# Kernel optimization log

Hardware: AMD Instinct MI355X
Metric: run time of the kernel (lower is better)

Reference implementation:

```python
import jax, jax.numpy as jnp
import numpy as np

D_MODEL = 1024
D_HIDDEN = 4096
BATCH = 4
SEQ = 2048
EPS = 1e-5
SLOPE = 0.01  # LeakyReLU default negative_slope


def layer_norm(x, g, b):
    m = jnp.mean(x, axis=-1, keepdims=True)
    v = jnp.mean(jnp.square(x - m), axis=-1, keepdims=True)
    return (x - m) * jax.lax.rsqrt(v + EPS) * g + b


def leaky_relu(x):
    return jnp.where(x >= 0, x, SLOPE * x)


def setup_inputs() -> dict:
    key = jax.random.key(0)
    ks = jax.random.split(key, 8)
    scale = D_MODEL ** 0.5
    x = jax.random.normal(ks[0], (BATCH, SEQ, D_MODEL), dtype=jnp.float32)
    qk = jax.random.normal(ks[1], (D_MODEL, D_MODEL), dtype=jnp.float32) / scale
    ov = jax.random.normal(ks[2], (D_MODEL, D_MODEL), dtype=jnp.float32) / scale
    ln1_g = jnp.ones((D_MODEL,), jnp.float32)
    ln1_b = jnp.zeros((D_MODEL,), jnp.float32)
    ln2_g = jnp.ones((D_MODEL,), jnp.float32)
    ln2_b = jnp.zeros((D_MODEL,), jnp.float32)
    # nn.Linear default init: uniform(-1/sqrt(fan_in), 1/sqrt(fan_in))
    def lin(k, fan_in, fan_out):
        k1, k2 = jax.random.split(k)
        bd = 1.0 / np.sqrt(fan_in)
        W = jax.random.uniform(k1, (fan_out, fan_in), jnp.float32, -bd, bd)
        b = jax.random.uniform(k2, (fan_out,), jnp.float32, -bd, bd)
        return W, b
    W_up, b_up = lin(ks[3], D_MODEL, D_HIDDEN)
    W_h, b_h = lin(ks[4], D_HIDDEN, D_HIDDEN)
    W_down, b_down = lin(ks[5], D_HIDDEN, D_MODEL)
    return {"x": x, "qk": qk, "ov": ov, "ln1_g": ln1_g, "ln1_b": ln1_b,
            "ln2_g": ln2_g, "ln2_b": ln2_b, "W_up": W_up, "b_up": b_up,
            "W_h": W_h, "b_h": b_h, "W_down": W_down, "b_down": b_down}


def reference(x, qk, ov, ln1_g, ln1_b, ln2_g, ln2_b,
              W_up, b_up, W_h, b_h, W_down, b_down):
    scale = D_MODEL ** 0.5
    # --- attention on ln1(x) ---
    h = layer_norm(x, ln1_g, ln1_b)                     # [B,S,D]
    scores = jnp.einsum('bsd,de,bte->bst', h, qk, h) / scale  # [B,S,S]
    n = h.shape[1]
    causal = jnp.tril(jnp.ones((n, n), bool))
    scores = jnp.where(causal, scores, -jnp.inf)
    probs = jax.nn.softmax(scores, axis=-1)
    attn = jnp.einsum('bst,btd,de->bse', probs, h, ov)  # [B,S,D]
    x = x + attn
    # --- MLP on ln2(x) ---
    h2 = layer_norm(x, ln2_g, ln2_b)
    a = leaky_relu(h2 @ W_up.T + b_up)
    a = leaky_relu(a @ W_h.T + b_h)
    a = leaky_relu(a @ W_down.T + b_down)
    return x + a
```

## Files before the change

### kernel.cpp

```cpp
#include <hip/hip_runtime.h>
#include <stdint.h>


typedef __attribute__((ext_vector_type(4))) float  f32x4;
typedef __attribute__((ext_vector_type(8))) __bf16 bf16v8;
typedef __attribute__((ext_vector_type(8))) unsigned short u16x8;
typedef unsigned short ushort_t;
typedef unsigned int   u32;

#define SLOPE 0.01f

__device__ __forceinline__ ushort_t f2bf(float f) {
  u32 u = __builtin_bit_cast(u32, f);
  u32 r = (u + 0x7FFFu + ((u >> 16) & 1u)) >> 16;
  return (ushort_t)r;
}
__device__ __forceinline__ float bf2f(ushort_t b) {
  u32 u = ((u32)b) << 16;
  return __builtin_bit_cast(float, u);
}

__device__ __forceinline__ void gload_lds16(const void* g, void* l) {
  __builtin_amdgcn_global_load_lds(
      (const __attribute__((address_space(1))) u32*)g,
      (__attribute__((address_space(3))) u32*)l, 16, 0, 0);
}

template<int EPI>
__global__ __launch_bounds__(512, 1)
void gemm_nt8(const ushort_t* __restrict__ A, const ushort_t* __restrict__ B,
              void* __restrict__ Cv, const float* __restrict__ bias,
              int M, int N, int K)
{
  extern __shared__ char smem[];
  const ushort_t* lds = (const ushort_t*)smem;
  const int tid = threadIdx.x;
  const int l   = tid & 63;
  const int m0 = blockIdx.y * 256;
  const int n0 = blockIdx.x * 256;
  const int wid = tid >> 6;
  const int wm = (wid >> 2) * 128;
  const int wn = (wid & 3) * 64;
  const int nt = K >> 6;

  const int  sg      = (((tid & 3) ^ ((tid >> 3) & 3))) * 8;
  const long rowA0   = (long)(m0 +       (tid >> 2)) * K;
  const long rowA1   = (long)(m0 + 128 + (tid >> 2)) * K;
  const long rowB0   = (long)(n0 +       (tid >> 2)) * K;
  const long rowB1   = (long)(n0 + 128 + (tid >> 2)) * K;
  const int  wbase16 = (tid & ~63) * 16;

#define STAGE_BOTH(TT) do {                                                   \
    const int  _buf = (TT) & 1;                                               \
    const long _k   = (long)(TT) * 64;                                        \
    char* _ra0 = (char*)smem + (_buf * 4 + 0) * 16384 + wbase16;              \
    char* _ra1 = (char*)smem + (_buf * 4 + 1) * 16384 + wbase16;              \
    char* _rb0 = (char*)smem + (_buf * 4 + 2) * 16384 + wbase16;              \
    char* _rb1 = (char*)smem + (_buf * 4 + 3) * 16384 + wbase16;              \
    gload_lds16(A + rowA0 + _k + sg,      _ra0);                              \
    gload_lds16(A + rowA1 + _k + sg,      _ra0 + 8192);                       \
    gload_lds16(B + rowB0 + _k + sg,      _rb0);                              \
    gload_lds16(B + rowB1 + _k + sg,      _rb0 + 8192);                       \
    gload_lds16(A + rowA0 + _k + 32 + sg, _ra1);                              \
    gload_lds16(A + rowA1 + _k + 32 + sg, _ra1 + 8192);                       \
    gload_lds16(B + rowB0 + _k + 32 + sg, _rb1);                              \
    gload_lds16(B + rowB1 + _k + 32 + sg, _rb1 + 8192);                       \
  } while (0)

  const int fr  = l & 15;
  const int fsl = (((l >> 4) ^ ((l >> 1) & 3))) * 8;

  f32x4 acc[8][4] = {};

  STAGE_BOTH(0);
  asm volatile("s_waitcnt vmcnt(4)" ::: "memory");
  __builtin_amdgcn_s_barrier();
  __builtin_amdgcn_sched_barrier(0);

  for (int t = 0; t < nt; ++t) {
    const int buf = t & 1;

    {
      const ushort_t* rA = lds + (buf * 4 + 0) * 8192 + (wm + fr) * 32 + fsl;
      const ushort_t* rB = lds + (buf * 4 + 2) * 8192 + (wn + fr) * 32 + fsl;
      bf16v8 av[8], bv[4];
#pragma unroll
      for (int mf = 0; mf < 8; mf++) av[mf] = *(const bf16v8*)(rA + mf * 512);
#pragma unroll
      for (int nf = 0; nf < 4; nf++) bv[nf] = *(const bf16v8*)(rB + nf * 512);

      if (t + 1 < nt) STAGE_BOTH(t + 1);

      __builtin_amdgcn_s_setprio(1);
#pragma unroll
      for (int mf = 0; mf < 8; mf++)
#pragma unroll
        for (int nf = 0; nf < 4; nf++)
          acc[mf][nf] = __builtin_amdgcn_mfma_f32_16x16x32_bf16(
              av[mf], bv[nf], acc[mf][nf], 0, 0, 0);
      __builtin_amdgcn_s_setprio(0);

      if (t + 1 < nt) {
        asm volatile("s_waitcnt vmcnt(8)" ::: "memory");
      } else {
        asm volatile("s_waitcnt vmcnt(0)" ::: "memory");
      }
      __builtin_amdgcn_s_barrier();
      __builtin_amdgcn_sched_barrier(0);
    }

    {
      const ushort_t* rA = lds + (buf * 4 + 1) * 8192 + (wm + fr) * 32 + fsl;
      const ushort_t* rB = lds + (buf * 4 + 3) * 8192 + (wn + fr) * 32 + fsl;
      bf16v8 av[8], bv[4];
#pragma unroll
      for (int mf = 0; mf < 8; mf++) av[mf] = *(const bf16v8*)(rA + mf * 512);
#pragma unroll
      for (int nf = 0; nf < 4; nf++) bv[nf] = *(const bf16v8*)(rB + nf * 512);

      __builtin_amdgcn_s_setprio(1);
#pragma unroll
      for (int mf = 0; mf < 8; mf++)
#pragma unroll
        for (int nf = 0; nf < 4; nf++)
          acc[mf][nf] = __builtin_amdgcn_mfma_f32_16x16x32_bf16(
              av[mf], bv[nf], acc[mf][nf], 0, 0, 0);
      __builtin_amdgcn_s_setprio(0);

      if (t + 1 < nt) {
        asm volatile("s_waitcnt vmcnt(4)" ::: "memory");
        __builtin_amdgcn_s_barrier();
        __builtin_amdgcn_sched_barrier(0);
      }
    }
  }
#undef STAGE_BOTH

  const int lr = (l >> 4) * 4;
#pragma unroll
  for (int mf = 0; mf < 8; mf++) {
    const int row0 = m0 + wm + mf * 16 + lr;
#pragma unroll
    for (int nf = 0; nf < 4; nf++) {
      const int col = n0 + wn + nf * 16 + fr;
      const float bcol = bias ? bias[col] : 0.f;
#pragma unroll
      for (int r = 0; r < 4; r++) {
        float v = acc[mf][nf][r];
        if constexpr (EPI == 2) {
          v += bcol;
          v = v >= 0.f ? v : SLOPE * v;
          ((ushort_t*)Cv)[(long)(row0 + r) * N + col] = f2bf(v);
        } else {
          ((ushort_t*)Cv)[(long)(row0 + r) * N + col] = f2bf(v);
        }
      }
    }
  }
}

template<int EPI, bool CAUSAL, bool KLIM>
__global__ __launch_bounds__(256)
void gemm_nt(const ushort_t* __restrict__ A, const ushort_t* __restrict__ B,
             void* __restrict__ Cv, const float* __restrict__ bias,
             const float* __restrict__ resid,
             int M, int N, int K, long sAb, long sBb, long sCb)
{
  __shared__ ushort_t lA[128 * 32];
  __shared__ ushort_t lB[128 * 32];
  const int tid = threadIdx.x;
  const int w = tid >> 6;
  const int l = tid & 63;
  const int m0 = blockIdx.y * 128;
  const int n0 = blockIdx.x * 128;
  if (CAUSAL && n0 > m0 + 127) return;
  const long bz = blockIdx.z;
  A += bz * sAb;
  B += bz * sBb;
  int Keff = K;
  if (KLIM) Keff = min(K, m0 + 128);

  const ushort_t* gA = A + (long)(m0 + w * 32 + (l >> 2)) * K + (l & 3) * 8;
  const ushort_t* gB = B + (long)(n0 + w * 32 + (l >> 2)) * K + (l & 3) * 8;
  ushort_t* lAw0 = &lA[(w * 32) * 32];
  ushort_t* lAw1 = &lA[(w * 32 + 16) * 32];
  ushort_t* lBw0 = &lB[(w * 32) * 32];
  ushort_t* lBw1 = &lB[(w * 32 + 16) * 32];
  const int wm = (w >> 1) * 64, wn = (w & 1) * 64;

  f32x4 acc[4][4] = {};

  for (int k0 = 0; k0 < Keff; k0 += 32) {
    gload_lds16(gA,                 lAw0);
    gload_lds16(gA + (long)16 * K,  lAw1);
    gload_lds16(gB,                 lBw0);
    gload_lds16(gB + (long)16 * K,  lBw1);
    gA += 32; gB += 32;
    __syncthreads();

    bf16v8 af[4], bfr[4];
#pragma unroll
    for (int m = 0; m < 4; m++)
      af[m] = *(const bf16v8*)&lA[(wm + m * 16 + (l & 15)) * 32 + (l >> 4) * 8];
#pragma unroll
    for (int n = 0; n < 4; n++)
      bfr[n] = *(const bf16v8*)&lB[(wn + n * 16 + (l & 15)) * 32 + (l >> 4) * 8];
#pragma unroll
    for (int m = 0; m < 4; m++)
#pragma unroll
      for (int n = 0; n < 4; n++)
        acc[m][n] = __builtin_amdgcn_mfma_f32_16x16x32_bf16(af[m], bfr[n], acc[m][n], 0, 0, 0);
    __syncthreads();
  }

  const int lr = (l >> 4) * 4;
  const int lc = l & 15;
#pragma unroll
  for (int m = 0; m < 4; m++) {
    const int row0 = m0 + wm + m * 16 + lr;
#pragma unroll
    for (int n = 0; n < 4; n++) {
      const int col = n0 + wn + n * 16 + lc;
#pragma unroll
      for (int r = 0; r < 4; r++) {
        float v = acc[m][n][r];
        const long idx = bz * sCb + (long)(row0 + r) * N + col;
        if constexpr (EPI == 0) {
          ((ushort_t*)Cv)[idx] = f2bf(v);
        } else if constexpr (EPI == 2) {
          v += bias[col];
          v = v >= 0.f ? v : SLOPE * v;
          ((ushort_t*)Cv)[idx] = f2bf(v);
        } else if constexpr (EPI == 3) {
          ((float*)Cv)[idx] = v + resid[idx];
        } else {
          v += bias[col];
          v = v >= 0.f ? v : SLOPE * v;
          ((float*)Cv)[idx] = v + resid[idx];
        }
      }
    }
  }
}

__global__ __launch_bounds__(256)
void ln_kernel(const float* __restrict__ x, const float* __restrict__ g,
               const float* __restrict__ bta, ushort_t* __restrict__ o)
{
  const long row = blockIdx.x;
  const int tid = threadIdx.x;
  const float4 v = *((const float4*)(x + row * 1024) + tid);
  float s  = v.x + v.y + v.z + v.w;
  float ss = v.x * v.x + v.y * v.y + v.z * v.z + v.w * v.w;
  for (int o2 = 32; o2 > 0; o2 >>= 1) {
    s  += __shfl_down(s, o2);
    ss += __shfl_down(ss, o2);
  }
  __shared__ float rs[4], rss[4];
  const int w = tid >> 6, l = tid & 63;
  if (l == 0) { rs[w] = s; rss[w] = ss; }
  __syncthreads();
  if (tid == 0) {
    float a = 0, c = 0;
    for (int i = 0; i < 4; i++) { a += rs[i]; c += rss[i]; }
    rs[0] = a; rss[0] = c;
  }
  __syncthreads();
  const float mean = rs[0] * (1.f / 1024.f);
  const float var  = rss[0] * (1.f / 1024.f) - mean * mean;
  const float rstd = rsqrtf(var + 1e-5f);
  const int c0 = tid * 4;
  ushort_t* orow = o + row * 1024;
  const float* vp = (const float*)&v;
#pragma unroll
  for (int i = 0; i < 4; i++)
    orow[c0 + i] = f2bf((vp[i] - mean) * rstd * g[c0 + i] + bta[c0 + i]);
}

__global__ __launch_bounds__(256)
void softmax_kernel(ushort_t* __restrict__ sc)
{
  const long row = blockIdx.x;
  const int s = (int)(row & 2047);
  const int tid = threadIdx.x;
  ushort_t* srow = sc + row * 2048;
  const int t0 = tid * 8;
  u16x8 raw = *(const u16x8*)(srow + t0);
  float v[8];
  const float rsc = 1.0f / 32.0f;
  float mx = -3e38f;
#pragma unroll
  for (int i = 0; i < 8; i++) {
    float f = bf2f(raw[i]) * rsc;
    v[i] = (t0 + i <= s) ? f : -3e38f;
    mx = fmaxf(mx, v[i]);
  }
  for (int o = 32; o > 0; o >>= 1) mx = fmaxf(mx, __shfl_down(mx, o));
  __shared__ float red[8];
  const int w = tid >> 6, l = tid & 63;
  if (l == 0) red[w] = mx;
  __syncthreads();
  if (tid == 0) {
    float m2 = red[0];
    for (int i = 1; i < 4; i++) m2 = fmaxf(m2, red[i]);
    red[0] = m2;
  }
  __syncthreads();
  const float m = red[0];
  float sum = 0.f;
#pragma unroll
  for (int i = 0; i < 8; i++) {
    float e = (t0 + i <= s) ? __expf(v[i] - m) : 0.f;
    v[i] = e; sum += e;
  }
  for (int o = 32; o > 0; o >>= 1) sum += __shfl_down(sum, o);
  if (l == 0) red[4 + w] = sum;
  __syncthreads();
  if (tid == 0) {
    float s2 = 0;
    for (int i = 0; i < 4; i++) s2 += red[4 + i];
    red[0] = 1.0f / s2;
  }
  __syncthreads();
  const float inv = red[0];
#pragma unroll
  for (int i = 0; i < 8; i++) srow[t0 + i] = f2bf(v[i] * inv);
}

__global__ __launch_bounds__(256)
void cast3_bf16(const float* __restrict__ a, const float* __restrict__ b,
                const float* __restrict__ c, ushort_t* __restrict__ oa,
                ushort_t* __restrict__ ob, ushort_t* __restrict__ oc)
{
  long i = ((long)blockIdx.x * 256 + threadIdx.x) * 4;
  const float* src; ushort_t* dst;
  if (i < 4194304L)        { src = a; dst = oa; }
  else if (i < 8388608L)   { src = b + (0 - 4194304L); dst = ob - 4194304L; }
  else                     { src = c + (0 - 8388608L); dst = oc - 8388608L; }
  float4 v = *(const float4*)(src + i);
  dst[i]     = f2bf(v.x);
  dst[i + 1] = f2bf(v.y);
  dst[i + 2] = f2bf(v.z);
  dst[i + 3] = f2bf(v.w);
}

__global__ __launch_bounds__(256)
void transpose_cast2(const float* __restrict__ s0, ushort_t* __restrict__ d0,
                     const float* __restrict__ s1, ushort_t* __restrict__ d1)
{
  __shared__ ushort_t t[32][33];
  const float* in = blockIdx.z ? s1 : s0;
  ushort_t*    o  = blockIdx.z ? d1 : d0;
  const int tx = threadIdx.x & 31, ty = threadIdx.x >> 5;
  const int r0 = blockIdx.y * 32, c0 = blockIdx.x * 32;
#pragma unroll
  for (int i = 0; i < 4; i++)
    t[ty + i * 8][tx] = f2bf(in[(long)(r0 + ty + i * 8) * 1024 + c0 + tx]);
  __syncthreads();
#pragma unroll
  for (int i = 0; i < 4; i++)
    o[(long)(c0 + ty + i * 8) * 1024 + r0 + tx] = t[tx][ty + i * 8];
}

__global__ __launch_bounds__(256)
void transpose_bf16(const ushort_t* __restrict__ in, ushort_t* __restrict__ o,
                    int R, int C)
{
  __shared__ ushort_t t[32][33];
  const long bz = blockIdx.z;
  in += bz * (long)R * C;
  o  += bz * (long)R * C;
  const int tx = threadIdx.x & 31, ty = threadIdx.x >> 5;
  const int r0 = blockIdx.y * 32, c0 = blockIdx.x * 32;
#pragma unroll
  for (int i = 0; i < 4; i++)
    t[ty + i * 8][tx] = in[(long)(r0 + ty + i * 8) * C + c0 + tx];
  __syncthreads();
#pragma unroll
  for (int i = 0; i < 4; i++)
    o[(long)(c0 + ty + i * 8) * R + r0 + tx] = t[tx][ty + i * 8];
}

extern "C" void kernel_launch(void* const* d_in, const int* in_sizes, int n_in,
                              void* d_out, int out_size, void* d_ws, size_t ws_size,
                              hipStream_t stream)
{
  const float* x      = (const float*)d_in[0];
  const float* qk     = (const float*)d_in[1];
  const float* ov     = (const float*)d_in[2];
  const float* ln1_g  = (const float*)d_in[3];
  const float* ln1_b  = (const float*)d_in[4];
  const float* ln2_g  = (const float*)d_in[5];
  const float* ln2_b  = (const float*)d_in[6];
  const float* W_up   = (const float*)d_in[7];
  const float* b_up   = (const float*)d_in[8];
  const float* W_h    = (const float*)d_in[9];
  const float* b_h    = (const float*)d_in[10];
  const float* W_down = (const float*)d_in[11];
  const float* b_down = (const float*)d_in[12];
  float* out = (float*)d_out;
  char* ws = (char*)d_ws;
  const long MB = 1024L * 1024L;

  ushort_t* wqT    = (ushort_t*)(ws +   0 * MB);
  ushort_t* woT    = (ushort_t*)(ws +   2 * MB);
  ushort_t* h      = (ushort_t*)(ws +   4 * MB);
  ushort_t* hT     = (ushort_t*)(ws +  20 * MB);
  ushort_t* q      = (ushort_t*)(ws +  36 * MB);
  ushort_t* scores = (ushort_t*)(ws +  52 * MB);
  ushort_t* h2     = h;
  ushort_t* attnh  = q;
  ushort_t* wu     = hT;
  ushort_t* wd     = (ushort_t*)(ws +  28 * MB);
  ushort_t* wh     = q;
  ushort_t* a1c    = (ushort_t*)(ws +  68 * MB);
  ushort_t* a2     = (ushort_t*)(ws + 100 * MB);

  const bool bigws = ws_size >= (size_t)(166 * MB);

  transpose_cast2<<<dim3(32, 32, 2), 256, 0, stream>>>(qk, wqT, ov, woT);
  ln_kernel<<<8192, 256, 0, stream>>>(x, ln1_g, ln1_b, h);
  transpose_bf16<<<dim3(32, 64, 4), 256, 0, stream>>>(h, hT, 2048, 1024);

  gemm_nt<0, false, false><<<dim3(8, 64, 1), 256, 0, stream>>>(
      h, wqT, q, nullptr, nullptr, 8192, 1024, 1024, 0, 0, 0);
  gemm_nt<0, true, false><<<dim3(16, 16, 4), 256, 0, stream>>>(
      q, h, scores, nullptr, nullptr, 2048, 2048, 1024,
      2048L * 1024, 2048L * 1024, 2048L * 2048);
  softmax_kernel<<<8192, 256, 0, stream>>>(scores);
  gemm_nt<0, false, true><<<dim3(8, 16, 4), 256, 0, stream>>>(
      scores, hT, attnh, nullptr, nullptr, 2048, 1024, 2048,
      2048L * 2048, 1024L * 2048, 2048L * 1024);
  gemm_nt<3, false, false><<<dim3(8, 64, 1), 256, 0, stream>>>(
      attnh, woT, out, nullptr, x, 8192, 1024, 1024, 0, 0, 0);

  ln_kernel<<<8192, 256, 0, stream>>>(out, ln2_g, ln2_b, h2);
  cast3_bf16<<<24576, 256, 0, stream>>>(W_up, W_down, W_h, wu, wd, wh);

  if (bigws) {
    for (int c = 0; c < 2; c++) {
      const long r0 = (long)c * 4096;
      gemm_nt8<2><<<dim3(16, 16, 1), 512, 131072, stream>>>(
          h2 + r0 * 1024, wu, a1c, b_up, 4096, 4096, 1024);
      gemm_nt8<2><<<dim3(16, 16, 1), 512, 131072, stream>>>(
          a1c, wh, a2 + r0 * 4096, b_h, 4096, 4096, 4096);
    }
    gemm_nt<4, false, false><<<dim3(8, 64, 1), 256, 0, stream>>>(
        a2, wd, out, b_down, out, 8192, 1024, 4096, 0, 0, 0);
  } else {
    for (int c = 0; c < 2; c++) {
      const long r0 = (long)c * 4096;
      gemm_nt8<2><<<dim3(16, 16, 1), 512, 131072, stream>>>(
          h2 + r0 * 1024, wu, a1c, b_up, 4096, 4096, 1024);
      gemm_nt8<2><<<dim3(16, 16, 1), 512, 131072, stream>>>(
          a1c, wh, a2, b_h, 4096, 4096, 4096);
      gemm_nt<4, false, false><<<dim3(8, 32, 1), 256, 0, stream>>>(
          a2, wd, out + r0 * 1024, b_down, out + r0 * 1024, 4096, 1024, 4096, 0, 0, 0);
    }
  }
}
```

Baseline: 707.9 us.

## Restructure GEMM mainloop into 4-buffer ring with 3-stage prefetch

Replaces the double-buffered 64-wide K step (two 32-wide halves per iteration) with a ring of four 32-wide LDS slots, issuing loads three tiles ahead. The aim is to hide global-to-LDS latency better by keeping more loads in flight. The price is one barrier per 32-K step instead of per half step, more complex tail waitcnt logic, and the same total LDS footprint of 128KB.

```diff
diff --git a/kernel.cpp b/kernel.cpp
--- a/kernel.cpp
+++ b/kernel.cpp
@@ -41,7 +41,7 @@
   const int wid = tid >> 6;
   const int wm = (wid >> 2) * 128;
   const int wn = (wid & 3) * 64;
-  const int nt = K >> 6;
+  const int nt = K >> 5;
 
   const int  sg      = (((tid & 3) ^ ((tid >> 3) & 3))) * 8;
   const long rowA0   = (long)(m0 +       (tid >> 2)) * K;
@@ -50,21 +50,14 @@
   const long rowB1   = (long)(n0 + 128 + (tid >> 2)) * K;
   const int  wbase16 = (tid & ~63) * 16;
 
-#define STAGE_BOTH(TT) do {                                                   \
-    const int  _buf = (TT) & 1;                                               \
-    const long _k   = (long)(TT) * 64;                                        \
-    char* _ra0 = (char*)smem + (_buf * 4 + 0) * 16384 + wbase16;              \
-    char* _ra1 = (char*)smem + (_buf * 4 + 1) * 16384 + wbase16;              \
-    char* _rb0 = (char*)smem + (_buf * 4 + 2) * 16384 + wbase16;              \
-    char* _rb1 = (char*)smem + (_buf * 4 + 3) * 16384 + wbase16;              \
-    gload_lds16(A + rowA0 + _k + sg,      _ra0);                              \
-    gload_lds16(A + rowA1 + _k + sg,      _ra0 + 8192);                       \
-    gload_lds16(B + rowB0 + _k + sg,      _rb0);                              \
-    gload_lds16(B + rowB1 + _k + sg,      _rb0 + 8192);                       \
-    gload_lds16(A + rowA0 + _k + 32 + sg, _ra1);                              \
-    gload_lds16(A + rowA1 + _k + 32 + sg, _ra1 + 8192);                       \
-    gload_lds16(B + rowB0 + _k + 32 + sg, _rb1);                              \
-    gload_lds16(B + rowB1 + _k + 32 + sg, _rb1 + 8192);                       \
+#define STAGE(TT) do {                                                        \
+    const long _k  = (long)(TT) * 32;                                         \
+    char* _ra = (char*)smem + ((TT) & 3) * 32768 + wbase16;                   \
+    char* _rb = _ra + 16384;                                                  \
+    gload_lds16(A + rowA0 + _k + sg, _ra);                                    \
+    gload_lds16(A + rowA1 + _k + sg, _ra + 8192);                             \
+    gload_lds16(B + rowB0 + _k + sg, _rb);                                    \
+    gload_lds16(B + rowB1 + _k + sg, _rb + 8192);                             \
   } while (0)
 
   const int fr  = l & 15;
@@ -72,69 +65,51 @@
 
   f32x4 acc[8][4] = {};
 
-  STAGE_BOTH(0);
-  asm volatile("s_waitcnt vmcnt(4)" ::: "memory");
+  STAGE(0);
+  if (nt > 1) STAGE(1);
+  if (nt > 2) STAGE(2);
+  if (nt > 2)      { asm volatile("s_waitcnt vmcnt(8)" ::: "memory"); }
+  else if (nt > 1) { asm volatile("s_waitcnt vmcnt(4)" ::: "memory"); }
+  else             { asm volatile("s_waitcnt vmcnt(0)" ::: "memory"); }
   __builtin_amdgcn_s_barrier();
   __builtin_amdgcn_sched_barrier(0);
 
   for (int t = 0; t < nt; ++t) {
-    const int buf = t & 1;
-
-    {
-      const ushort_t* rA = lds + (buf * 4 + 0) * 8192 + (wm + fr) * 32 + fsl;
-      const ushort_t* rB = lds + (buf * 4 + 2) * 8192 + (wn + fr) * 32 + fsl;
-      bf16v8 av[8], bv[4];
-#pragma unroll
-      for (int mf = 0; mf < 8; mf++) av[mf] = *(const bf16v8*)(rA + mf * 512);
-#pragma unroll
-      for (int nf = 0; nf < 4; nf++) bv[nf] = *(const bf16v8*)(rB + nf * 512);
-
-      if (t + 1 < nt) STAGE_BOTH(t + 1);
-
-      __builtin_amdgcn_s_setprio(1);
-#pragma unroll
-      for (int mf = 0; mf < 8; mf++)
-#pragma unroll
-        for (int nf = 0; nf < 4; nf++)
-          acc[mf][nf] = __builtin_amdgcn_mfma_f32_16x16x32_bf16(
-              av[mf], bv[nf], acc[mf][nf], 0, 0, 0);
-      __builtin_amdgcn_s_setprio(0);
-
-      if (t + 1 < nt) {
-        asm volatile("s_waitcnt vmcnt(8)" ::: "memory");
-      } else {
-        asm volatile("s_waitcnt vmcnt(0)" ::: "memory");
-      }
+    const int buf = t & 3;
+    const ushort_t* rA = lds + buf * 16384 +        (wm + fr) * 32 + fsl;
+    const ushort_t* rB = lds + buf * 16384 + 8192 + (wn + fr) * 32 + fsl;
+    bf16v8 av[8], bv[4];
+#pragma unroll
+    for (int mf = 0; mf < 8; mf++) av[mf] = *(const bf16v8*)(rA + mf * 512);
+#pragma unroll
+    for (int nf = 0; nf < 4; nf++) bv[nf] = *(const bf16v8*)(rB + nf * 512);
+
+    if (t + 3 < nt) STAGE(t + 3);
+
+    __builtin_amdgcn_s_setprio(1);
+#pragma unroll
+    for (int mf = 0; mf < 8; mf++)
+#pragma unroll
+      for (int nf = 0; nf < 4; nf++)
+        acc[mf][nf] = __builtin_amdgcn_mfma_f32_16x16x32_bf16(
+            av[mf], bv[nf], acc[mf][nf], 0, 0, 0);
+    __builtin_amdgcn_s_setprio(0);
+
+    if (t <= nt - 4) {
+      asm volatile("s_waitcnt vmcnt(8)" ::: "memory");
+      __builtin_amdgcn_s_barrier();
+      __builtin_amdgcn_sched_barrier(0);
+    } else if (t == nt - 3) {
+      asm volatile("s_waitcnt vmcnt(4)" ::: "memory");
+      __builtin_amdgcn_s_barrier();
+      __builtin_amdgcn_sched_barrier(0);
+    } else if (t == nt - 2) {
+      asm volatile("s_waitcnt vmcnt(0)" ::: "memory");
       __builtin_amdgcn_s_barrier();
       __builtin_amdgcn_sched_barrier(0);
     }
-
-    {
-      const ushort_t* rA = lds + (buf * 4 + 1) * 8192 + (wm + fr) * 32 + fsl;
-      const ushort_t* rB = lds + (buf * 4 + 3) * 8192 + (wn + fr) * 32 + fsl;
-      bf16v8 av[8], bv[4];
-#pragma unroll
-      for (int mf = 0; mf < 8; mf++) av[mf] = *(const bf16v8*)(rA + mf * 512);
-#pragma unroll
-      for (int nf = 0; nf < 4; nf++) bv[nf] = *(const bf16v8*)(rB + nf * 512);
-
-      __builtin_amdgcn_s_setprio(1);
-#pragma unroll
-      for (int mf = 0; mf < 8; mf++)
-#pragma unroll
-        for (int nf = 0; nf < 4; nf++)
-          acc[mf][nf] = __builtin_amdgcn_mfma_f32_16x16x32_bf16(
-              av[mf], bv[nf], acc[mf][nf], 0, 0, 0);
-      __builtin_amdgcn_s_setprio(0);
-
-      if (t + 1 < nt) {
-        asm volatile("s_waitcnt vmcnt(4)" ::: "memory");
-        __builtin_amdgcn_s_barrier();
-        __builtin_amdgcn_sched_barrier(0);
-      }
-    }
-  }
-#undef STAGE_BOTH
+  }
+#undef STAGE
 
   const int lr = (l >> 4) * 4;
 #pragma unroll
```

Measured after the change: 685.0 us. 3.2% less time.
